# Performance work log

Hardware: AMD Instinct MI355X
Metric: run time of the kernel (lower is better)

The kernel has to match this reference:

```python
import jax, jax.numpy as jnp
import numpy as np

NUM_NODES = 80000
V_GLOBALS = 50000
N = 32      # grapharea_size
D = 300     # feature dim
R = 4       # num relations
E = 64      # edges per timestep
B, T = 2, 64


def setup_inputs() -> dict:
    key = jax.random.key(0)
    ks = jax.random.split(key, 10)
    return {
        "x_indices": jax.random.randint(ks[0], (B, T, N), 0, NUM_NODES, dtype=jnp.int32),
        "edge_index": jax.random.randint(ks[1], (B, T, 2, E), 0, N, dtype=jnp.int32),
        "edge_type": jax.random.randint(ks[2], (B, T, E), 0, R, dtype=jnp.int32),
        "X": jax.random.normal(ks[3], (NUM_NODES, D), jnp.float32) * 0.1,
        "conv_W": jax.random.normal(ks[4], (R, D, D), jnp.float32) * (1.0 / np.sqrt(D)),
        "W_0": jax.random.normal(ks[5], (D, D), jnp.float32) * (1.0 / np.sqrt(D)),
        "update_gate_W": jax.random.normal(ks[6], (N * D, D), jnp.float32) * (1.0 / np.sqrt(N * D)),
        "update_gate_U": jax.random.normal(ks[7], (D, D), jnp.float32) * (1.0 / np.sqrt(D)),
        "lin_w": jax.random.normal(ks[8], (V_GLOBALS, D), jnp.float32) * (1.0 / np.sqrt(D)),
        "lin_b": jax.random.normal(ks[9], (V_GLOBALS,), jnp.float32) * 0.01,
    }


def _rgcn_step(X, conv_W, W_0, Wg, Ug, lin_w, lin_b, mem, idx, ei, et):
    # gather grapharea features: [N, D]
    gx = X[idx]
    src, dst = ei[0], ei[1]
    n = gx.shape[0]
    r = conv_W.shape[0]
    # per-relation linear transform: [R, N, D]
    xw = jnp.einsum('nd,rde->rne', gx, conv_W)
    # edge-type masks emulate split_edge_index: [R, E]
    mask = (et[None, :] == jnp.arange(r, dtype=et.dtype)[:, None]).astype(gx.dtype)
    # GCN symmetric normalization with self-loops (deg includes self-loop weight 1)
    deg = jax.vmap(lambda w: jax.ops.segment_sum(w, dst, num_segments=n))(mask) + 1.0  # [R, N]
    dis = jax.lax.rsqrt(deg)
    norm = dis[:, src] * dis[:, dst] * mask                      # [R, E]
    msgs = xw[:, src, :] * norm[..., None]                       # [R, E, D]
    agg = jax.vmap(lambda m: jax.ops.segment_sum(m, dst, num_segments=n))(msgs)
    agg = agg + xw * (dis ** 2)[..., None]                       # self-loop messages
    composite = agg.sum(0)                                       # sum over relations, [N, D]
    # eye(N) @ (gx @ W_0) == gx @ W_0
    proposed = composite + gx @ W_0
    # GRU-style update gate from flattened grapharea + previous memory's first node
    u = jax.nn.sigmoid(gx.reshape(-1) @ Wg + mem[0] @ Ug)        # [D]
    new = u[None, :] * proposed + (1.0 - u[None, :]) * mem       # [N, D]
    x1 = jax.nn.leaky_relu(new)[0]                               # current node, [D]
    logits = x1 @ lin_w.T + lin_b                                # [V]
    return new, jax.nn.log_softmax(logits)


def reference(x_indices, edge_index, edge_type, X, conv_W, W_0, update_gate_W, update_gate_U, lin_w, lin_b):
    b, t, n = x_indices.shape
    s = b * t
    idxs = x_indices.reshape(s, n)
    eis = edge_index.reshape(s, 2, -1)
    ets = edge_type.reshape(s, -1)

    def step(mem, inp):
        idx, ei, et = inp
        new, logp = _rgcn_step(X, conv_W, W_0, update_gate_W, update_gate_U,
                               lin_w, lin_b, mem, idx, ei, et)
        # memory carry is a non-grad buffer updated via .data.copy_ in torch
        return jax.lax.stop_gradient(new), logp

    mem0 = jnp.zeros((n, X.shape[1]), X.dtype)
    _, preds_globals = jax.lax.scan(step, mem0, (idxs, eis, ets))  # [S, V]
    preds_senses = jnp.zeros((s,), X.dtype)  # include_senses=False -> stacked zeros
    return preds_globals, preds_senses
```

## Files before the change

### kernel.cpp

```cpp
#include <hip/hip_runtime.h>

#define S 128
#define N 32
#define D 300
#define DP 320
#define E 64
#define R 4
#define V 50000
#define VP 50048
#define ND 9600
#define KY 1504
#define DPAD 304

typedef unsigned short ushortT;
typedef __attribute__((ext_vector_type(8))) short short8;
typedef __attribute__((ext_vector_type(4))) short short4v;
typedef __attribute__((ext_vector_type(4))) float floatx4;
typedef __attribute__((ext_vector_type(2))) float floatx2;
typedef __attribute__((ext_vector_type(2))) _Float16 half2v;
typedef __attribute__((ext_vector_type(13))) unsigned int uintx13;

#if defined(__has_builtin)
#if __has_builtin(__builtin_amdgcn_fdot2)
#define HAVE_FDOT2 1
#endif
#endif

__device__ inline float bf2f(ushortT h) {
    unsigned u = ((unsigned)h) << 16;
    float f;
    __builtin_memcpy(&f, &u, 4);
    return f;
}

__device__ inline float bfbits_lo(unsigned u) {
    unsigned b = u << 16;
    float f;
    __builtin_memcpy(&f, &b, 4);
    return f;
}

__device__ inline float bfbits_hi(unsigned u) {
    unsigned b = u & 0xffff0000u;
    float f;
    __builtin_memcpy(&f, &b, 4);
    return f;
}

__device__ inline ushortT f2bf(float f) {
    unsigned u;
    __builtin_memcpy(&u, &f, 4);
    unsigned r = (u + 0x7fffu + ((u >> 16) & 1u)) >> 16;
    return (ushortT)r;
}

__device__ inline float ldf(const void* p, size_t i, int isb) {
    return isb ? bf2f(((const ushortT*)p)[i]) : ((const float*)p)[i];
}

__device__ inline float dot2f(unsigned a, unsigned b, float c) {
    half2v av, bv;
    __builtin_memcpy(&av, &a, 4);
    __builtin_memcpy(&bv, &b, 4);
#if defined(HAVE_FDOT2)
    return __builtin_amdgcn_fdot2(av, bv, c, false);
#else
    return fmaf((float)av[1], (float)bv[1], fmaf((float)av[0], (float)bv[0], c));
#endif
}

__device__ inline unsigned packh2(float lo, float hi) {
    half2v h;
    h[0] = (_Float16)lo;
    h[1] = (_Float16)hi;
    unsigned u;
    __builtin_memcpy(&u, &h, 4);
    return u;
}

__global__ void k_detect(const void* X, int* flag) {
    __shared__ int bad;
    if (threadIdx.x == 0) bad = 0;
    __syncthreads();
    const ushortT* p = (const ushortT*)X;
    int b = 0;
    for (int i = threadIdx.x; i < 4096; i += 256) {
        float v = bf2f(p[i]);
        if (!(v > -2.f && v < 2.f)) b = 1;
    }
    if (b) atomicOr(&bad, 1);
    __syncthreads();
    if (threadIdx.x == 0) flag[0] = bad ? 0 : 1;
}

__global__ void k_prep(const int* __restrict__ flag, const void* __restrict__ Wg,
                       const void* __restrict__ convW, const void* __restrict__ W0,
                       ushortT* __restrict__ wgt, ushortT* __restrict__ wst) {
    int isb = flag[0];
    __shared__ float tile[32][33];
    int bx = blockIdx.x;
    int d0 = blockIdx.y * 32;
    int tx = threadIdx.x & 31, ty = threadIdx.x >> 5;
    if (bx < ND / 32) {
        int k0 = bx * 32;
        for (int i = ty; i < 32; i += 8) {
            int d = d0 + tx;
            tile[i][tx] = (d < D) ? ldf(Wg, (size_t)(k0 + i) * D + d, isb) : 0.f;
        }
        __syncthreads();
        for (int i = ty; i < 32; i += 8) {
            int d = d0 + i;
            if (d < DPAD) wgt[(size_t)d * ND + k0 + tx] = f2bf(tile[tx][i]);
        }
    } else {
        int k0 = (bx - ND / 32) * 32;
        for (int i = ty; i < 32; i += 8) {
            int kp = k0 + i, d = d0 + tx;
            float v = 0.f;
            if (d < D && kp < 1500)
                v = (kp < 1200) ? ldf(convW, (size_t)kp * D + d, isb)
                                : ldf(W0, (size_t)(kp - 1200) * D + d, isb);
            tile[i][tx] = v;
        }
        __syncthreads();
        for (int i = ty; i < 32; i += 8) {
            int d = d0 + i;
            if (d < DPAD) wst[(size_t)d * KY + k0 + tx] = f2bf(tile[tx][i]);
        }
    }
}

__global__ void k_gyb(const int* __restrict__ flag, const int* __restrict__ xi,
                      const void* __restrict__ X, const int* __restrict__ ei,
                      const int* __restrict__ et, ushortT* __restrict__ gxb,
                      ushortT* __restrict__ yb) {
    int isb = flag[0];
    int s = blockIdx.x;
    int t = threadIdx.x;
    __shared__ ushortT gl[N][D];
    __shared__ int se[E], de[E], te[E];
    __shared__ float disv[R][N];
    if (t < E) {
        se[t] = ei[(size_t)s * 2 * E + t];
        de[t] = ei[(size_t)s * 2 * E + E + t];
        te[t] = et[(size_t)s * E + t];
    }
    if (t < D) {
#pragma unroll 4
        for (int r = 0; r < N; ++r) {
            int node = xi[s * N + r];
            ushortT v = isb ? ((const ushortT*)X)[(size_t)node * D + t]
                            : f2bf(((const float*)X)[(size_t)node * D + t]);
            gl[r][t] = v;
            gxb[(size_t)(s * N + r) * D + t] = v;
        }
    }
    __syncthreads();
    if (t < R * N) {
        int r = t >> 5, n = t & 31;
        float c = 1.f;
        for (int e = 0; e < E; ++e) c += (te[e] == r && de[e] == n) ? 1.f : 0.f;
        disv[r][n] = rsqrtf(c);
    }
    __syncthreads();
    if (t < D) {
        float g0 = bf2f(gl[0][t]);
        float yy[R];
#pragma unroll
        for (int r = 0; r < R; ++r) yy[r] = g0 * disv[r][0] * disv[r][0];
        for (int e = 0; e < E; ++e) {
            if (de[e] == 0) {
                int r = te[e];
                yy[r] += disv[r][se[e]] * disv[r][0] * bf2f(gl[se[e]][t]);
            }
        }
#pragma unroll
        for (int r = 0; r < R; ++r) yb[(size_t)s * KY + r * D + t] = f2bf(yy[r]);
        yb[(size_t)s * KY + 4 * D + t] = gl[0][t];
    }
    if (t < 4) yb[(size_t)s * KY + 1500 + t] = 0;
}

__global__ __launch_bounds__(256) void k_gemm2(const ushortT* __restrict__ gxb,
                                               const ushortT* __restrict__ wgt,
                                               const ushortT* __restrict__ yb,
                                               const ushortT* __restrict__ wst,
                                               float* __restrict__ apart,
                                               float* __restrict__ ppart, int nza, int nzp) {
    int wave = threadIdx.x >> 6, lane = threadIdx.x & 63;
    int col = lane & 15, quad = lane >> 4;
    int m0 = blockIdx.x * 16, n0 = blockIdx.y * 16;
    int z = blockIdx.z;
    const ushortT *A, *Bt;
    float* C;
    int ld, kchunks, per, zz;
    if (z < nza) {
        A = gxb; Bt = wgt; C = apart; ld = ND; kchunks = ND / 32;
        zz = z; per = (kchunks + nza - 1) / nza;
    } else {
        A = yb; Bt = wst; C = ppart; ld = KY; kchunks = KY / 32;
        zz = z - nza; per = (kchunks + nzp - 1) / nzp;
    }
    int kbeg = zz * per;
    int kend = kbeg + per;
    if (kend > kchunks) kend = kchunks;
    floatx4 acc = {0.f, 0.f, 0.f, 0.f};
    const ushortT* ap = A + (size_t)(m0 + col) * ld + quad * 8;
    const ushortT* bp = Bt + (size_t)(n0 + col) * ld + quad * 8;
    for (int kc = kbeg + wave; kc < kend; kc += 4) {
        short8 a = *(const short8*)(ap + kc * 32);
        short8 b = *(const short8*)(bp + kc * 32);
        acc = __builtin_amdgcn_mfma_f32_16x16x32_bf16(a, b, acc, 0, 0, 0);
    }
    __shared__ float red[4][64][4];
#pragma unroll
    for (int i = 0; i < 4; ++i) red[wave][lane][i] = acc[i];
    __syncthreads();
    if (wave == 0) {
#pragma unroll
        for (int i = 0; i < 4; ++i) {
            float v = red[0][lane][i] + red[1][lane][i] + red[2][lane][i] + red[3][lane][i];
            int m = m0 + quad * 4 + i;
            int n = n0 + col;
            if (n < D) C[(size_t)zz * S * D + (size_t)m * D + n] = v;
        }
    }
}

__global__ void k_red2(const float* __restrict__ apart, const float* __restrict__ ppart,
                       float* __restrict__ a, float* __restrict__ P0, int nza, int nzp) {
    int i = blockIdx.x * 256 + threadIdx.x;
    if (i < S * D) {
        float v = 0.f;
        for (int z = 0; z < nza; ++z) v += apart[(size_t)z * S * D + i];
        a[i] = v;
        float w = 0.f;
        for (int z = 0; z < nzp; ++z) w += ppart[(size_t)z * S * D + i];
        P0[i] = w;
    }
}

__global__ __attribute__((amdgpu_flat_work_group_size(768, 768), amdgpu_waves_per_eu(2, 2))) void
k_scan(const int* __restrict__ flag, const float* __restrict__ a, const float* __restrict__ P0,
       const void* __restrict__ Ug, ushortT* __restrict__ x1p) {
    int isb = flag[0];
    int t = threadIdx.x;
    int w = t >> 6, lane = t & 63;
    int kbase = w * 25;
    int myk = kbase + lane;
    bool red_ok = lane < 25;
    int d4 = 256 + lane;
    bool d4ok = d4 < D;
    uintx13 UV0, UV1, UV2, UV3, UV4;
#pragma unroll
    for (int j = 0; j < 13; ++j) {
        int k1 = kbase + 2 * j, k2 = k1 + 1;
        bool k2ok = (2 * j + 1) < 25;
        UV0[j] = packh2(ldf(Ug, (size_t)k1 * D + lane, isb),
                        k2ok ? ldf(Ug, (size_t)k2 * D + lane, isb) : 0.f);
        UV1[j] = packh2(ldf(Ug, (size_t)k1 * D + 64 + lane, isb),
                        k2ok ? ldf(Ug, (size_t)k2 * D + 64 + lane, isb) : 0.f);
        UV2[j] = packh2(ldf(Ug, (size_t)k1 * D + 128 + lane, isb),
                        k2ok ? ldf(Ug, (size_t)k2 * D + 128 + lane, isb) : 0.f);
        UV3[j] = packh2(ldf(Ug, (size_t)k1 * D + 192 + lane, isb),
                        k2ok ? ldf(Ug, (size_t)k2 * D + 192 + lane, isb) : 0.f);
        UV4[j] = packh2(d4ok ? ldf(Ug, (size_t)k1 * D + d4, isb) : 0.f,
                        (k2ok && d4ok) ? ldf(Ug, (size_t)k2 * D + d4, isb) : 0.f);
    }
    for (int i = t; i < S * 20; i += 768) {
        int s = i / 20, d = 300 + (i % 20);
        x1p[(size_t)s * DP + d] = 0;
    }
    __shared__ float part[2][12][320];
    __shared__ unsigned msh16[12 * 13];
    for (int i = t; i < 12 * 13; i += 768) msh16[i] = 0;
    float mreg = 0.f;
    int buf = 0;
    float av = 0.f, pv = 0.f;
    if (red_ok) {
        av = a[myk];
        pv = P0[myk];
    }
    __syncthreads();
    for (int s = 0; s < S; ++s) {
        float avn = 0.f, pvn = 0.f;
        if (red_ok && s + 1 < S) {
            avn = a[(size_t)(s + 1) * D + myk];
            pvn = P0[(size_t)(s + 1) * D + myk];
        }
        uintx13 MV;
#pragma unroll
        for (int j = 0; j < 13; ++j) MV[j] = msh16[13 * w + j];
        float acc0 = 0.f, acc1 = 0.f, acc2 = 0.f, acc3 = 0.f, acc4 = 0.f;
#pragma unroll
        for (int j = 0; j < 13; ++j) {
            unsigned md = MV[j];
            acc0 = dot2f(UV0[j], md, acc0);
            acc1 = dot2f(UV1[j], md, acc1);
            acc2 = dot2f(UV2[j], md, acc2);
            acc3 = dot2f(UV3[j], md, acc3);
            acc4 = dot2f(UV4[j], md, acc4);
        }
        part[buf][w][lane] = acc0;
        part[buf][w][64 + lane] = acc1;
        part[buf][w][128 + lane] = acc2;
        part[buf][w][192 + lane] = acc3;
        part[buf][w][256 + lane] = acc4;
        __builtin_amdgcn_sched_barrier(0);
        asm volatile("s_waitcnt lgkmcnt(0)" ::: "memory");
        __builtin_amdgcn_s_barrier();
        __builtin_amdgcn_sched_barrier(0);
        if (red_ok) {
            float q0 = part[buf][0][myk] + part[buf][1][myk];
            float q1 = part[buf][2][myk] + part[buf][3][myk];
            float q2 = part[buf][4][myk] + part[buf][5][myk];
            float q3 = part[buf][6][myk] + part[buf][7][myk];
            float q4 = part[buf][8][myk] + part[buf][9][myk];
            float q5 = part[buf][10][myk] + part[buf][11][myk];
            float pr = av + (((q0 + q1) + (q2 + q3)) + (q4 + q5));
            float u = 1.f / (1.f + __expf(-pr));
            float nm = u * pv + (1.f - u) * mreg;
            mreg = nm;
            _Float16 mh = (_Float16)nm;
            ushortT mb;
            __builtin_memcpy(&mb, &mh, 2);
            ((ushortT*)msh16)[26 * w + lane] = mb;
            float x = nm > 0.f ? nm : 0.01f * nm;
            x1p[(size_t)s * DP + myk] = f2bf(x);
        }
        av = avn;
        pv = pvn;
        buf ^= 1;
    }
}

__global__ __launch_bounds__(256) void k_logits(const int* __restrict__ flag,
                                                const ushortT* __restrict__ x1p,
                                                const void* __restrict__ lw,
                                                const void* __restrict__ lb,
                                                void* __restrict__ out) {
    int isb = flag[0];
    int wave = threadIdx.x >> 6, lane = threadIdx.x & 63;
    int col = lane & 15, quad = lane >> 4;
    int v = blockIdx.x * 64 + wave * 16 + col;
    int vv = v < V ? v : V - 1;
    floatx4 acc[8];
#pragma unroll
    for (int i = 0; i < 8; ++i) acc[i] = (floatx4){0.f, 0.f, 0.f, 0.f};
#pragma unroll
    for (int kc = 0; kc < 9; ++kc) {
        int k0 = kc * 32 + quad * 8;
        short8 b;
        if (isb) {
            const ushortT* bp = (const ushortT*)lw + (size_t)vv * D + k0;
            short4v lo = *(const short4v*)bp;
            short4v hi = *(const short4v*)(bp + 4);
            b = (short8){lo[0], lo[1], lo[2], lo[3], hi[0], hi[1], hi[2], hi[3]};
        } else {
            const float* bp = (const float*)lw + (size_t)vv * D + k0;
            floatx4 f0 = *(const floatx4*)bp;
            floatx4 f1 = *(const floatx4*)(bp + 4);
            b = (short8){(short)f2bf(f0[0]), (short)f2bf(f0[1]), (short)f2bf(f0[2]),
                         (short)f2bf(f0[3]), (short)f2bf(f1[0]), (short)f2bf(f1[1]),
                         (short)f2bf(f1[2]), (short)f2bf(f1[3])};
        }
#pragma unroll
        for (int st = 0; st < 8; ++st) {
            short8 aa = *(const short8*)(x1p + (size_t)(st * 16 + col) * DP + k0);
            acc[st] = __builtin_amdgcn_mfma_f32_16x16x32_bf16(aa, b, acc[st], 0, 0, 0);
        }
    }
    {
        int k0 = 288 + quad * 8;
        short8 b;
#pragma unroll
        for (int j = 0; j < 8; ++j) {
            int k = k0 + j;
            ushortT bv = 0;
            if (k < D)
                bv = isb ? ((const ushortT*)lw)[(size_t)vv * D + k]
                         : f2bf(((const float*)lw)[(size_t)vv * D + k]);
            b[j] = (short)bv;
        }
#pragma unroll
        for (int st = 0; st < 8; ++st) {
            short8 aa = *(const short8*)(x1p + (size_t)(st * 16 + col) * DP + k0);
            acc[st] = __builtin_amdgcn_mfma_f32_16x16x32_bf16(aa, b, acc[st], 0, 0, 0);
        }
    }
    if (v < V) {
        float bias = ldf(lb, v, isb);
#pragma unroll
        for (int st = 0; st < 8; ++st) {
#pragma unroll
            for (int i = 0; i < 4; ++i) {
                int s = st * 16 + quad * 4 + i;
                float val = acc[st][i] + bias;
                if (isb)
                    ((ushortT*)out)[(size_t)s * V + v] = f2bf(val);
                else
                    ((float*)out)[(size_t)s * V + v] = val;
            }
        }
    }
}

__global__ __launch_bounds__(512) void k_norm(const int* __restrict__ flag,
                                              void* __restrict__ out) {
    int isb = flag[0];
    int s = blockIdx.x;
    int t = threadIdx.x;
    __shared__ float red[512];
    if (s == 0 && t < S) {
        if (isb)
            ((ushortT*)out)[(size_t)S * V + t] = 0;
        else
            ((float*)out)[(size_t)S * V + t] = 0.f;
    }
    float mx = -1e30f;
    if (isb) {
        const uint4* row = (const uint4*)((const ushortT*)out + (size_t)s * V);
        for (int i = t; i < 6250; i += 512) {
            uint4 q = row[i];
            mx = fmaxf(mx, fmaxf(fmaxf(bfbits_lo(q.x), bfbits_hi(q.x)),
                                 fmaxf(bfbits_lo(q.y), bfbits_hi(q.y))));
            mx = fmaxf(mx, fmaxf(fmaxf(bfbits_lo(q.z), bfbits_hi(q.z)),
                                 fmaxf(bfbits_lo(q.w), bfbits_hi(q.w))));
        }
    } else {
        const floatx4* row = (const floatx4*)((const float*)out + (size_t)s * V);
        for (int i = t; i < 12500; i += 512) {
            floatx4 q = row[i];
            mx = fmaxf(mx, fmaxf(fmaxf(q[0], q[1]), fmaxf(q[2], q[3])));
        }
    }
    red[t] = mx;
    __syncthreads();
    for (int o = 256; o > 0; o >>= 1) {
        if (t < o) red[t] = fmaxf(red[t], red[t + o]);
        __syncthreads();
    }
    float M = red[0];
    __syncthreads();
    float sm = 0.f;
    if (isb) {
        const uint4* row = (const uint4*)((const ushortT*)out + (size_t)s * V);
        for (int i = t; i < 6250; i += 512) {
            uint4 q = row[i];
            sm += __expf(bfbits_lo(q.x) - M) + __expf(bfbits_hi(q.x) - M) +
                  __expf(bfbits_lo(q.y) - M) + __expf(bfbits_hi(q.y) - M) +
                  __expf(bfbits_lo(q.z) - M) + __expf(bfbits_hi(q.z) - M) +
                  __expf(bfbits_lo(q.w) - M) + __expf(bfbits_hi(q.w) - M);
        }
    } else {
        const floatx4* row = (const floatx4*)((const float*)out + (size_t)s * V);
        for (int i = t; i < 12500; i += 512) {
            floatx4 q = row[i];
            sm += __expf(q[0] - M) + __expf(q[1] - M) + __expf(q[2] - M) + __expf(q[3] - M);
        }
    }
    red[t] = sm;
    __syncthreads();
    for (int o = 256; o > 0; o >>= 1) {
        if (t < o) red[t] += red[t + o];
        __syncthreads();
    }
    float lse = M + __logf(red[0]);
    if (isb) {
        uint4* row = (uint4*)((ushortT*)out + (size_t)s * V);
        for (int i = t; i < 6250; i += 512) {
            uint4 q = row[i];
            uint4 o;
            o.x = (unsigned)f2bf(bfbits_lo(q.x) - lse) |
                  ((unsigned)f2bf(bfbits_hi(q.x) - lse) << 16);
            o.y = (unsigned)f2bf(bfbits_lo(q.y) - lse) |
                  ((unsigned)f2bf(bfbits_hi(q.y) - lse) << 16);
            o.z = (unsigned)f2bf(bfbits_lo(q.z) - lse) |
                  ((unsigned)f2bf(bfbits_hi(q.z) - lse) << 16);
            o.w = (unsigned)f2bf(bfbits_lo(q.w) - lse) |
                  ((unsigned)f2bf(bfbits_hi(q.w) - lse) << 16);
            row[i] = o;
        }
    } else {
        floatx4* row = (floatx4*)((float*)out + (size_t)s * V);
        for (int i = t; i < 12500; i += 512) {
            floatx4 q = row[i];
            q[0] -= lse;
            q[1] -= lse;
            q[2] -= lse;
            q[3] -= lse;
            row[i] = q;
        }
    }
}

#define OFF_FLAG 0
#define OFF_GXB 256
#define OFF_WGT 2457856
#define OFF_WST 8294656
#define OFF_YB 9209088
#define OFF_A 9594112
#define OFF_P0 9747712
#define OFF_X1P 9901312
#define OFF_STATS 9983232
#define OFF_PART 9983744
#define PART_A_BYTES (4 * S * D * 4)
#define PART_P_BYTES (2 * S * D * 4)

extern "C" void kernel_launch(void* const* d_in, const int* in_sizes, int n_in, void* d_out,
                              int out_size, void* d_ws, size_t ws_size, hipStream_t stream) {
    const int* xi = (const int*)d_in[0];
    const int* ei = (const int*)d_in[1];
    const int* et = (const int*)d_in[2];
    const void* X = d_in[3];
    const void* convW = d_in[4];
    const void* W0 = d_in[5];
    const void* Wg = d_in[6];
    const void* Ug = d_in[7];
    const void* lw = d_in[8];
    const void* lb = d_in[9];
    char* ws = (char*)d_ws;

    int* flag = (int*)(ws + OFF_FLAG);
    ushortT* gxb = (ushortT*)(ws + OFF_GXB);
    ushortT* wgt = (ushortT*)(ws + OFF_WGT);
    ushortT* wst = (ushortT*)(ws + OFF_WST);
    ushortT* yb = (ushortT*)(ws + OFF_YB);
    float* a = (float*)(ws + OFF_A);
    float* P0 = (float*)(ws + OFF_P0);
    ushortT* x1p = (ushortT*)(ws + OFF_X1P);

    bool split = ws_size >= (size_t)(OFF_PART + PART_A_BYTES + PART_P_BYTES);
    int nza = split ? 4 : 1;
    int nzp = split ? 2 : 1;
    float* apart = split ? (float*)(ws + OFF_PART) : a;
    float* ppart = split ? (float*)(ws + OFF_PART + PART_A_BYTES) : P0;

    hipLaunchKernelGGL(k_detect, dim3(1), dim3(256), 0, stream, X, flag);
    hipLaunchKernelGGL(k_prep, dim3(ND / 32 + KY / 32, 10), dim3(256), 0, stream, flag, Wg,
                       convW, W0, wgt, wst);
    hipLaunchKernelGGL(k_gyb, dim3(S), dim3(DP), 0, stream, flag, xi, X, ei, et, gxb, yb);
    hipLaunchKernelGGL(k_gemm2, dim3(S / 16, 19, nza + nzp), dim3(256), 0, stream, gxb, wgt,
                       yb, wst, apart, ppart, nza, nzp);
    if (split)
        hipLaunchKernelGGL(k_red2, dim3((S * D + 255) / 256), dim3(256), 0, stream, apart,
                           ppart, a, P0, nza, nzp);
    hipLaunchKernelGGL(k_scan, dim3(1), dim3(768), 0, stream, flag, a, P0, Ug, x1p);
    hipLaunchKernelGGL(k_logits, dim3(VP / 64), dim3(256), 0, stream, flag, x1p, lw, lb, d_out);
    hipLaunchKernelGGL(k_norm, dim3(S), dim3(512), 0, stream, flag, d_out);
}
```

Baseline: 423.9 us.

## Compute sequential GRU gate matvec with MFMA instead of fdot2 partial sums

Rewrites the serial 128-step scan kernel so the mem·Ug matvec uses 16x16x32 f16 MFMA tiles. Each wave owns one or two 16-column output slices, with Ug kept partly in registers and partly in LDS. The new memory row goes into a double-buffered A-tile image in LDS. This removes the cross-wave partial-sum reduction through shared memory and halves the work per step on the latency-bound critical path. In exchange it wastes 15 of 16 MFMA rows and adds LDS reads of the second Ug slice on every step.

```diff
diff --git a/kernel.cpp b/kernel.cpp
--- a/kernel.cpp
+++ b/kernel.cpp
@@ -16,15 +16,7 @@
 typedef __attribute__((ext_vector_type(8))) short short8;
 typedef __attribute__((ext_vector_type(4))) short short4v;
 typedef __attribute__((ext_vector_type(4))) float floatx4;
-typedef __attribute__((ext_vector_type(2))) float floatx2;
-typedef __attribute__((ext_vector_type(2))) _Float16 half2v;
-typedef __attribute__((ext_vector_type(13))) unsigned int uintx13;
-
-#if defined(__has_builtin)
-#if __has_builtin(__builtin_amdgcn_fdot2)
-#define HAVE_FDOT2 1
-#endif
-#endif
+typedef __attribute__((ext_vector_type(8))) _Float16 half8;
 
 __device__ inline float bf2f(ushortT h) {
     unsigned u = ((unsigned)h) << 16;
@@ -56,26 +48,6 @@
 
 __device__ inline float ldf(const void* p, size_t i, int isb) {
     return isb ? bf2f(((const ushortT*)p)[i]) : ((const float*)p)[i];
-}
-
-__device__ inline float dot2f(unsigned a, unsigned b, float c) {
-    half2v av, bv;
-    __builtin_memcpy(&av, &a, 4);
-    __builtin_memcpy(&bv, &b, 4);
-#if defined(HAVE_FDOT2)
-    return __builtin_amdgcn_fdot2(av, bv, c, false);
-#else
-    return fmaf((float)av[1], (float)bv[1], fmaf((float)av[0], (float)bv[0], c));
-#endif
-}
-
-__device__ inline unsigned packh2(float lo, float hi) {
-    half2v h;
-    h[0] = (_Float16)lo;
-    h[1] = (_Float16)hi;
-    unsigned u;
-    __builtin_memcpy(&u, &h, 4);
-    return u;
 }
 
 __global__ void k_detect(const void* X, int* flag) {
@@ -246,90 +218,104 @@
     int isb = flag[0];
     int t = threadIdx.x;
     int w = t >> 6, lane = t & 63;
-    int kbase = w * 25;
-    int myk = kbase + lane;
-    bool red_ok = lane < 25;
-    int d4 = 256 + lane;
-    bool d4ok = d4 < D;
-    uintx13 UV0, UV1, UV2, UV3, UV4;
-#pragma unroll
-    for (int j = 0; j < 13; ++j) {
-        int k1 = kbase + 2 * j, k2 = k1 + 1;
-        bool k2ok = (2 * j + 1) < 25;
-        UV0[j] = packh2(ldf(Ug, (size_t)k1 * D + lane, isb),
-                        k2ok ? ldf(Ug, (size_t)k2 * D + lane, isb) : 0.f);
-        UV1[j] = packh2(ldf(Ug, (size_t)k1 * D + 64 + lane, isb),
-                        k2ok ? ldf(Ug, (size_t)k2 * D + 64 + lane, isb) : 0.f);
-        UV2[j] = packh2(ldf(Ug, (size_t)k1 * D + 128 + lane, isb),
-                        k2ok ? ldf(Ug, (size_t)k2 * D + 128 + lane, isb) : 0.f);
-        UV3[j] = packh2(ldf(Ug, (size_t)k1 * D + 192 + lane, isb),
-                        k2ok ? ldf(Ug, (size_t)k2 * D + 192 + lane, isb) : 0.f);
-        UV4[j] = packh2(d4ok ? ldf(Ug, (size_t)k1 * D + d4, isb) : 0.f,
-                        (k2ok && d4ok) ? ldf(Ug, (size_t)k2 * D + d4, isb) : 0.f);
-    }
+    int quad = lane >> 4, col = lane & 15;
+    bool has2 = w < 7;
+    __shared__ _Float16 ug_lds[7][10][512];
+    __shared__ _Float16 aimg[2][10][512];
+    half8 ugr[10];
+#pragma unroll
+    for (int c = 0; c < 10; ++c) {
+        half8 v;
+#pragma unroll
+        for (int i = 0; i < 8; ++i) {
+            int k = c * 32 + quad * 8 + i;
+            int n = w * 16 + col;
+            v[i] = (_Float16)((k < D) ? ldf(Ug, (size_t)k * D + n, isb) : 0.f);
+        }
+        ugr[c] = v;
+    }
+    if (has2) {
+#pragma unroll
+        for (int c = 0; c < 10; ++c) {
+#pragma unroll
+            for (int i = 0; i < 8; ++i) {
+                int k = c * 32 + quad * 8 + i;
+                int n = (12 + w) * 16 + col;
+                ug_lds[w][c][lane * 8 + i] =
+                    (_Float16)((k < D && n < D) ? ldf(Ug, (size_t)k * D + n, isb) : 0.f);
+            }
+        }
+    }
+    for (int i = t; i < 2 * 10 * 512; i += 768) ((ushortT*)aimg)[i] = 0;
     for (int i = t; i < S * 20; i += 768) {
         int s = i / 20, d = 300 + (i % 20);
         x1p[(size_t)s * DP + d] = 0;
     }
-    __shared__ float part[2][12][320];
-    __shared__ unsigned msh16[12 * 13];
-    for (int i = t; i < 12 * 13; i += 768) msh16[i] = 0;
-    float mreg = 0.f;
+    bool ep = quad == 0;
+    int n1 = w * 16 + col;
+    int n2 = (12 + w) * 16 + col;
+    bool ep2 = ep && has2 && (n2 < D);
+    int wi1 = (n1 >> 5) * 512 + ((n1 >> 3) & 3) * 128 + (n1 & 7);
+    int wi2 = (n2 >> 5) * 512 + ((n2 >> 3) & 3) * 128 + (n2 & 7);
+    float m1 = 0.f, m2 = 0.f;
+    float av1 = 0.f, pv1 = 0.f, av2 = 0.f, pv2 = 0.f;
+    if (ep) {
+        av1 = a[n1];
+        pv1 = P0[n1];
+    }
+    if (ep2) {
+        av2 = a[n2];
+        pv2 = P0[n2];
+    }
+    __syncthreads();
     int buf = 0;
-    float av = 0.f, pv = 0.f;
-    if (red_ok) {
-        av = a[myk];
-        pv = P0[myk];
-    }
-    __syncthreads();
     for (int s = 0; s < S; ++s) {
-        float avn = 0.f, pvn = 0.f;
-        if (red_ok && s + 1 < S) {
-            avn = a[(size_t)(s + 1) * D + myk];
-            pvn = P0[(size_t)(s + 1) * D + myk];
-        }
-        uintx13 MV;
-#pragma unroll
-        for (int j = 0; j < 13; ++j) MV[j] = msh16[13 * w + j];
-        float acc0 = 0.f, acc1 = 0.f, acc2 = 0.f, acc3 = 0.f, acc4 = 0.f;
-#pragma unroll
-        for (int j = 0; j < 13; ++j) {
-            unsigned md = MV[j];
-            acc0 = dot2f(UV0[j], md, acc0);
-            acc1 = dot2f(UV1[j], md, acc1);
-            acc2 = dot2f(UV2[j], md, acc2);
-            acc3 = dot2f(UV3[j], md, acc3);
-            acc4 = dot2f(UV4[j], md, acc4);
-        }
-        part[buf][w][lane] = acc0;
-        part[buf][w][64 + lane] = acc1;
-        part[buf][w][128 + lane] = acc2;
-        part[buf][w][192 + lane] = acc3;
-        part[buf][w][256 + lane] = acc4;
+        float an1 = 0.f, pn1 = 0.f, an2 = 0.f, pn2 = 0.f;
+        if (ep && s + 1 < S) {
+            an1 = a[(size_t)(s + 1) * D + n1];
+            pn1 = P0[(size_t)(s + 1) * D + n1];
+        }
+        if (ep2 && s + 1 < S) {
+            an2 = a[(size_t)(s + 1) * D + n2];
+            pn2 = P0[(size_t)(s + 1) * D + n2];
+        }
+        floatx4 c1 = {0.f, 0.f, 0.f, 0.f};
+        floatx4 c2 = {0.f, 0.f, 0.f, 0.f};
+#pragma unroll
+        for (int c = 0; c < 10; ++c) {
+            half8 af = *(const half8*)&aimg[buf][c][lane * 8];
+            c1 = __builtin_amdgcn_mfma_f32_16x16x32_f16(af, ugr[c], c1, 0, 0, 0);
+            if (has2) {
+                half8 bf = *(const half8*)&ug_lds[w][c][lane * 8];
+                c2 = __builtin_amdgcn_mfma_f32_16x16x32_f16(af, bf, c2, 0, 0, 0);
+            }
+        }
+        if (ep) {
+            float pr = av1 + c1[0];
+            float u = 1.f / (1.f + __expf(-pr));
+            float nm = u * pv1 + (1.f - u) * m1;
+            m1 = nm;
+            ((_Float16*)aimg[buf ^ 1])[wi1] = (_Float16)nm;
+            float x = nm > 0.f ? nm : 0.01f * nm;
+            x1p[(size_t)s * DP + n1] = f2bf(x);
+        }
+        if (ep2) {
+            float pr = av2 + c2[0];
+            float u = 1.f / (1.f + __expf(-pr));
+            float nm = u * pv2 + (1.f - u) * m2;
+            m2 = nm;
+            ((_Float16*)aimg[buf ^ 1])[wi2] = (_Float16)nm;
+            float x = nm > 0.f ? nm : 0.01f * nm;
+            x1p[(size_t)s * DP + n2] = f2bf(x);
+        }
         __builtin_amdgcn_sched_barrier(0);
         asm volatile("s_waitcnt lgkmcnt(0)" ::: "memory");
         __builtin_amdgcn_s_barrier();
         __builtin_amdgcn_sched_barrier(0);
-        if (red_ok) {
-            float q0 = part[buf][0][myk] + part[buf][1][myk];
-            float q1 = part[buf][2][myk] + part[buf][3][myk];
-            float q2 = part[buf][4][myk] + part[buf][5][myk];
-            float q3 = part[buf][6][myk] + part[buf][7][myk];
-            float q4 = part[buf][8][myk] + part[buf][9][myk];
-            float q5 = part[buf][10][myk] + part[buf][11][myk];
-            float pr = av + (((q0 + q1) + (q2 + q3)) + (q4 + q5));
-            float u = 1.f / (1.f + __expf(-pr));
-            float nm = u * pv + (1.f - u) * mreg;
-            mreg = nm;
-            _Float16 mh = (_Float16)nm;
-            ushortT mb;
-            __builtin_memcpy(&mb, &mh, 2);
-            ((ushortT*)msh16)[26 * w + lane] = mb;
-            float x = nm > 0.f ? nm : 0.01f * nm;
-            x1p[(size_t)s * DP + myk] = f2bf(x);
-        }
-        av = avn;
-        pv = pvn;
+        av1 = an1;
+        pv1 = pn1;
+        av2 = an2;
+        pv2 = pn2;
         buf ^= 1;
     }
 }
```

After: 487.2 us. 1.15x slower.
